# Performance work log

Hardware: AMD Instinct MI355X
Metric: run time of the kernel (lower is better)

Reference implementation:

```python
import jax, jax.numpy as jnp
import numpy as np
import math

NUM_HEADS = 8
HEAD_SIZE = 32

def get_alibi_slopes(n_heads):
    def pow2_slopes(n):
        start = 2.0 ** (-2.0 ** (-(math.log2(n) - 3)))
        ratio = start
        return [start * ratio ** i for i in range(n)]
    if math.log2(n_heads).is_integer():
        return np.array(pow2_slopes(n_heads), dtype=np.float32)
    cp2 = 2 ** math.floor(math.log2(n_heads))
    extra = pow2_slopes(2 * cp2)[0::2][: n_heads - cp2]
    return np.array(pow2_slopes(cp2) + extra, dtype=np.float32)

ALIBI_SLOPES = jnp.asarray(get_alibi_slopes(NUM_HEADS))  # [H]

def setup_inputs() -> dict:
    key = jax.random.key(0)
    ks = jax.random.split(key, 6)
    B, T, C = 32, 512, 256
    s = 1.0 / math.sqrt(C)
    return {
        "x": jax.random.normal(ks[0], (B, T, C), dtype=jnp.float32),
        "Wq": jax.random.normal(ks[1], (C, NUM_HEADS * HEAD_SIZE), dtype=jnp.float32) * s,
        "Wk": jax.random.normal(ks[2], (C, NUM_HEADS * HEAD_SIZE), dtype=jnp.float32) * s,
        "Wv": jax.random.normal(ks[3], (C, NUM_HEADS * HEAD_SIZE), dtype=jnp.float32) * s,
        "Wo": jax.random.normal(ks[4], (NUM_HEADS * HEAD_SIZE, C), dtype=jnp.float32) * s,
        "bo": jax.random.normal(ks[5], (C,), dtype=jnp.float32) * 0.01,
    }

def reference(x, Wq, Wk, Wv, Wo, bo):
    # Faithful eval-mode forward (dropout disabled) of the torch MultiHeadAttention.
    B, T, C = x.shape
    H, D = NUM_HEADS, HEAD_SIZE
    q = (x @ Wq).reshape(B, T, H, D).transpose(0, 2, 1, 3)  # [B,H,T,D]
    k = (x @ Wk).reshape(B, T, H, D).transpose(0, 2, 1, 3)
    v = (x @ Wv).reshape(B, T, H, D).transpose(0, 2, 1, 3)
    scale = 1.0 / math.sqrt(D)
    wei = jnp.einsum("bhtd,bhsd->bhts", q, k) * scale  # [B,H,T,T]
    pos = jnp.arange(T)
    rel = (pos[None, :] - pos[:, None]).astype(jnp.float32)  # bias[i,j] = j - i
    bias = ALIBI_SLOPES[:, None, None] * rel[None, :, :]      # [H,T,T]
    wei = wei + bias[None]
    causal = pos[None, :] <= pos[:, None]  # [T,T], True where j <= i
    wei = jnp.where(causal[None, None], wei, -jnp.inf)
    wei = jax.nn.softmax(wei, axis=-1)
    out = jnp.einsum("bhts,bhsd->bhtd", wei, v)  # [B,H,T,D]
    out = out.transpose(0, 2, 1, 3).reshape(B, T, H * D)
    return out @ Wo + bo
```

## Files before the change

### kernel.cpp

```cpp
#include <hip/hip_runtime.h>
#include <stdint.h>

#define LOG2E 1.4426950408889634f

typedef __attribute__((ext_vector_type(8))) short bf16x8;
typedef __attribute__((ext_vector_type(4))) float f32x4;

__device__ __forceinline__ unsigned short f2bf(float f) {
  union { float f; unsigned int u; } v; v.f = f;
  unsigned int u = v.u;
  u += 0x7FFFu + ((u >> 16) & 1u);
  return (unsigned short)(u >> 16);
}

__device__ __forceinline__ unsigned int cvt_pk_bf16(float lo, float hi) {
  unsigned int r;
  asm("v_cvt_pk_bf16_f32 %0, %1, %2" : "=v"(r) : "v"(lo), "v"(hi));
  return r;
}

__global__ void cvt_f32_bf16(const float* __restrict__ src, unsigned short* __restrict__ dst, int n4) {
  int i = blockIdx.x * blockDim.x + threadIdx.x;
  if (i < n4) {
    float4 v = reinterpret_cast<const float4*>(src)[i];
    ushort4 o;
    o.x = f2bf(v.x); o.y = f2bf(v.y); o.z = f2bf(v.z); o.w = f2bf(v.w);
    reinterpret_cast<ushort4*>(dst)[i] = o;
  }
}

struct WPtrs { const float* src[4]; unsigned short* dst[4]; };
__global__ void transpose_w(WPtrs p) {
  __shared__ float tile[32][33];
  const float* src = p.src[blockIdx.z];
  unsigned short* dst = p.dst[blockIdx.z];
  int x = blockIdx.x * 32 + threadIdx.x;
  int y = blockIdx.y * 32 + threadIdx.y;
  #pragma unroll
  for (int j = 0; j < 32; j += 8)
    tile[threadIdx.y + j][threadIdx.x] = src[(y + j) * 256 + x];
  __syncthreads();
  int xo = blockIdx.y * 32 + threadIdx.x;
  int yo = blockIdx.x * 32 + threadIdx.y;
  #pragma unroll
  for (int j = 0; j < 32; j += 8)
    dst[(yo + j) * 256 + xo] = f2bf(tile[threadIdx.x][threadIdx.y + j]);
}

template<int MODE>
__launch_bounds__(256, 2)
__global__ void gemm128(const unsigned short* __restrict__ A,
                        const unsigned short* __restrict__ Wt,
                        unsigned short* __restrict__ q_out,
                        unsigned short* __restrict__ k_out,
                        unsigned short* __restrict__ vT,
                        const float* __restrict__ bo,
                        float* __restrict__ f_out) {
  __shared__ unsigned short As[128][72];
  __shared__ unsigned short Bs[128][72];
  const int tid = threadIdx.x;
  const int m0 = blockIdx.x * 128;
  int wsel, n0;
  if (MODE == 0) { wsel = blockIdx.y >> 1; n0 = (blockIdx.y & 1) * 128; }
  else           { wsel = 0;               n0 = blockIdx.y * 128; }
  const unsigned short* W = Wt + wsel * 65536;
  const int w = tid >> 6, lane = tid & 63;
  const int wm = (w >> 1) * 64, wn = (w & 1) * 64;
  const int lr = lane & 15, lg = lane >> 4;

  f32x4 acc[4][4] = {};

  for (int kt = 0; kt < 4; ++kt) {
    #pragma unroll
    for (int cc = 0; cc < 4; ++cc) {
      int c = tid + cc * 256;
      int row = c >> 3, col = (c & 7) * 8;
      *reinterpret_cast<int4*>(&As[row][col]) =
        *reinterpret_cast<const int4*>(&A[(size_t)(m0 + row) * 256 + kt * 64 + col]);
      *reinterpret_cast<int4*>(&Bs[row][col]) =
        *reinterpret_cast<const int4*>(&W[(size_t)(n0 + row) * 256 + kt * 64 + col]);
    }
    __syncthreads();
    #pragma unroll
    for (int kk = 0; kk < 2; ++kk) {
      bf16x8 af[4], bfr[4];
      #pragma unroll
      for (int mf = 0; mf < 4; ++mf)
        af[mf] = *reinterpret_cast<const bf16x8*>(&As[wm + mf * 16 + lr][kk * 32 + lg * 8]);
      #pragma unroll
      for (int nf = 0; nf < 4; ++nf)
        bfr[nf] = *reinterpret_cast<const bf16x8*>(&Bs[wn + nf * 16 + lr][kk * 32 + lg * 8]);
      #pragma unroll
      for (int mf = 0; mf < 4; ++mf)
        #pragma unroll
        for (int nf = 0; nf < 4; ++nf)
          acc[mf][nf] = __builtin_amdgcn_mfma_f32_16x16x32_bf16(af[mf], bfr[nf], acc[mf][nf], 0, 0, 0);
    }
    __syncthreads();
  }

  if (MODE == 0) {
    if (wsel < 2) {
      unsigned short* dst = (wsel == 0) ? q_out : k_out;
      #pragma unroll
      for (int mf = 0; mf < 4; ++mf)
        #pragma unroll
        for (int nf = 0; nf < 4; ++nf)
          #pragma unroll
          for (int r = 0; r < 4; ++r)
            dst[(size_t)(m0 + wm + mf * 16 + lg * 4 + r) * 256 + (n0 + wn + nf * 16 + lr)] =
              f2bf(acc[mf][nf][r]);
    } else {
      #pragma unroll
      for (int mf = 0; mf < 4; ++mf)
        #pragma unroll
        for (int nf = 0; nf < 4; ++nf) {
          int ncol = n0 + wn + nf * 16 + lr;
          int h = ncol >> 5, d = ncol & 31;
          int m = m0 + wm + mf * 16 + lg * 4;
          int b = m >> 9, t = m & 511;
          ushort4 pk;
          pk.x = f2bf(acc[mf][nf][0]); pk.y = f2bf(acc[mf][nf][1]);
          pk.z = f2bf(acc[mf][nf][2]); pk.w = f2bf(acc[mf][nf][3]);
          *reinterpret_cast<ushort4*>(&vT[((size_t)((b * 8 + h) * 32 + d)) * 512 + t]) = pk;
        }
    }
  } else {
    #pragma unroll
    for (int mf = 0; mf < 4; ++mf)
      #pragma unroll
      for (int nf = 0; nf < 4; ++nf)
        #pragma unroll
        for (int r = 0; r < 4; ++r) {
          int ncol = n0 + wn + nf * 16 + lr;
          f_out[(size_t)(m0 + wm + mf * 16 + lg * 4 + r) * 256 + ncol] = acc[mf][nf][r] + bo[ncol];
        }
  }
}

__launch_bounds__(256, 2)
__global__ void attn_k(const unsigned short* __restrict__ qb,
                       const unsigned short* __restrict__ kb,
                       const unsigned short* __restrict__ vT,
                       unsigned short* __restrict__ ob) {
  extern __shared__ unsigned short smem[];
  unsigned short* Ks = smem;
  unsigned short* Vs = smem + 16384;
  unsigned short* Pl = smem + 32768;
  const int p = blockIdx.x, h = blockIdx.y, b = blockIdx.z;
  const int tid = threadIdx.x, wv = tid >> 6, lane = tid & 63;
  const int lr = lane & 15, lg = lane >> 4;

  {
    const unsigned short* ksrc = kb + ((size_t)b * 512) * 256 + h * 32;
    #pragma unroll
    for (int it = 0; it < 8; ++it) {
      int idx = tid + it * 256;
      int row = idx >> 2, g = idx & 3;
      *reinterpret_cast<int4*>(&Ks[row * 32 + g * 8]) =
        *reinterpret_cast<const int4*>(&ksrc[(size_t)row * 256 + g * 8]);
    }
    const unsigned short* vsrc = vT + ((size_t)(b * 8 + h) * 32) * 512;
    #pragma unroll
    for (int it = 0; it < 8; ++it) {
      int idx = tid + it * 256;
      int d = idx >> 6, cg = idx & 63;
      int col = (cg * 8) ^ ((d & 7) << 3);
      *reinterpret_cast<int4*>(&Vs[d * 512 + col]) =
        *reinterpret_cast<const int4*>(&vsrc[(size_t)d * 512 + cg * 8]);
    }
  }
  __syncthreads();

  const float scale2 = 0.17677669529663687f * LOG2E;
  const float slope2 = exp2f(-(float)(h + 1)) * LOG2E;
  float cc[16];
  #pragma unroll
  for (int t = 0; t < 4; ++t)
    #pragma unroll
    for (int r = 0; r < 4; ++r) cc[t * 4 + r] = slope2 * (float)(t * 16 + r);

  char* Plw = (char*)(Pl) + wv * 2048;
  const int swz = (lr & 7) << 4;

  for (int i = 0; i < 4; ++i) {
    const int c = p + 2 * (wv + 4 * i);
    const int qq = c * 16;
    bf16x8 qf = *reinterpret_cast<const bf16x8*>(
        &qb[((size_t)(b * 512 + qq + lr)) * 256 + h * 32 + lg * 8]);
    float m = -1e30f, l = 0.f;
    f32x4 oT0 = {0.f, 0.f, 0.f, 0.f}, oT1 = {0.f, 0.f, 0.f, 0.f};
    const int nsteps = c / 4 + 1;
    const int nfull = (qq >= 63) ? ((qq - 63) / 64 + 1) : 0;
    const float bb0 = slope2 * (float)(lg * 4 - lr - qq);

    for (int s = 0; s < nsteps; ++s) {
      const int kb0 = s * 64;
      f32x4 sv[4];
      #pragma unroll
      for (int t = 0; t < 4; ++t) {
        bf16x8 kf = *reinterpret_cast<const bf16x8*>(&Ks[(kb0 + t * 16 + lr) * 32 + lg * 8]);
        f32x4 z = {0.f, 0.f, 0.f, 0.f};
        sv[t] = __builtin_amdgcn_mfma_f32_16x16x32_bf16(kf, qf, z, 0, 0, 0);
      }
      float bb = bb0 + slope2 * (float)kb0;
      float x[16];
      #pragma unroll
      for (int t = 0; t < 4; ++t)
        #pragma unroll
        for (int r = 0; r < 4; ++r)
          x[t * 4 + r] = sv[t][r] * scale2 + (bb + cc[t * 4 + r]);
      if (s >= nfull) {
        int thr = qq + lr - kb0 - lg * 4;
        #pragma unroll
        for (int t = 0; t < 4; ++t)
          #pragma unroll
          for (int r = 0; r < 4; ++r)
            x[t * 4 + r] = ((t * 16 + r) <= thr) ? x[t * 4 + r] : -1e30f;
      }
      float bm = x[0];
      #pragma unroll
      for (int j = 1; j < 16; ++j) bm = fmaxf(bm, x[j]);
      bm = fmaxf(bm, __shfl_xor(bm, 16));
      bm = fmaxf(bm, __shfl_xor(bm, 32));
      float mn = fmaxf(m, bm);
      float alpha = __builtin_amdgcn_exp2f(m - mn);
      m = mn;
      l *= alpha;
      #pragma unroll
      for (int r = 0; r < 4; ++r) { oT0[r] *= alpha; oT1[r] *= alpha; }
      float ps = 0.f;
      #pragma unroll
      for (int j = 0; j < 16; ++j) { x[j] = __builtin_amdgcn_exp2f(x[j] - m); ps += x[j]; }
      l += ps;
      #pragma unroll
      for (int t = 0; t < 4; ++t)
        #pragma unroll
        for (int pp = 0; pp < 2; ++pp) {
          unsigned int w2 = cvt_pk_bf16(x[t * 4 + 2 * pp], x[t * 4 + 2 * pp + 1]);
          int cbyte = (t * 32 + lg * 8 + pp * 4) ^ swz;
          *reinterpret_cast<unsigned int*>(Plw + lr * 128 + cbyte) = w2;
        }
      #pragma unroll
      for (int ks = 0; ks < 2; ++ks) {
        int cb = (ks * 64 + lg * 16) ^ swz;
        bf16x8 pb = *reinterpret_cast<const bf16x8*>(Plw + lr * 128 + cb);
        #pragma unroll
        for (int dt = 0; dt < 2; ++dt) {
          int d = dt * 16 + lr;
          int col = (kb0 + ks * 32 + lg * 8) ^ ((d & 7) << 3);
          bf16x8 vf = *reinterpret_cast<const bf16x8*>(&Vs[d * 512 + col]);
          if (dt == 0) oT0 = __builtin_amdgcn_mfma_f32_16x16x32_bf16(vf, pb, oT0, 0, 0, 0);
          else         oT1 = __builtin_amdgcn_mfma_f32_16x16x32_bf16(vf, pb, oT1, 0, 0, 0);
        }
      }
    }
    l += __shfl_xor(l, 16);
    l += __shfl_xor(l, 32);
    float inv = 1.0f / l;
    unsigned int w0 = cvt_pk_bf16(oT0[0] * inv, oT0[1] * inv);
    unsigned int w1 = cvt_pk_bf16(oT0[2] * inv, oT0[3] * inv);
    unsigned int w2 = cvt_pk_bf16(oT1[0] * inv, oT1[1] * inv);
    unsigned int w3 = cvt_pk_bf16(oT1[2] * inv, oT1[3] * inv);
    size_t obase = ((size_t)(b * 512 + qq + lr)) * 256 + h * 32;
    *reinterpret_cast<uint2*>(&ob[obase + lg * 4]) = make_uint2(w0, w1);
    *reinterpret_cast<uint2*>(&ob[obase + 16 + lg * 4]) = make_uint2(w2, w3);
  }
}

extern "C" void kernel_launch(void* const* d_in, const int* in_sizes, int n_in,
                              void* d_out, int out_size, void* d_ws, size_t ws_size,
                              hipStream_t stream) {
  const float* x  = (const float*)d_in[0];
  const float* Wq = (const float*)d_in[1];
  const float* Wk = (const float*)d_in[2];
  const float* Wv = (const float*)d_in[3];
  const float* Wo = (const float*)d_in[4];
  const float* bo = (const float*)d_in[5];
  float* out = (float*)d_out;

  char* ws = (char*)d_ws;
  unsigned short* xb = (unsigned short*)(ws);
  unsigned short* qb = (unsigned short*)(ws + (8u  << 20));
  unsigned short* kb = (unsigned short*)(ws + (16u << 20));
  unsigned short* vT = (unsigned short*)(ws + (24u << 20));
  unsigned short* wt = (unsigned short*)(ws + (32u << 20));
  unsigned short* ob = xb;

  cvt_f32_bf16<<<4096, 256, 0, stream>>>(x, xb, 1048576);

  WPtrs p;
  p.src[0] = Wq; p.src[1] = Wk; p.src[2] = Wv; p.src[3] = Wo;
  p.dst[0] = wt; p.dst[1] = wt + 65536; p.dst[2] = wt + 2 * 65536; p.dst[3] = wt + 3 * 65536;
  transpose_w<<<dim3(8, 8, 4), dim3(32, 8), 0, stream>>>(p);

  gemm128<0><<<dim3(128, 6), 256, 0, stream>>>(xb, wt, qb, kb, vT, nullptr, nullptr);
  attn_k<<<dim3(2, 8, 32), 256, 73728, stream>>>(qb, kb, vT, ob);
  gemm128<1><<<dim3(128, 2), 256, 0, stream>>>(ob, wt + 3 * 65536, nullptr, nullptr, nullptr, bo, out);
}
```

Measured before the change: 63.64 us.

## Fuse x conversion into QKV GEMM, interleave attention chunks, swizzle K tiles

Removes the separate fp32-to-bf16 conversion kernel for x and converts inside the QKV GEMM tile load, saving one launch and one round trip of x through global memory. The attention kernel now gives each wave four query chunks paired so their causal lengths balance (g, 15-g, 16+g, 31-g) and steps them together, so multiple independent chains are in flight. K rows are stored in LDS with an XOR swizzle to cut bank conflicts, and the GEMM launch bounds rise to 3 blocks per CU. Keeping four chunk states live raises register pressure, and the QKV GEMM now reads fp32 x, doubling its A-tile global traffic.

```diff
diff --git a/kernel.cpp b/kernel.cpp
--- a/kernel.cpp
+++ b/kernel.cpp
@@ -17,16 +17,6 @@
   unsigned int r;
   asm("v_cvt_pk_bf16_f32 %0, %1, %2" : "=v"(r) : "v"(lo), "v"(hi));
   return r;
-}
-
-__global__ void cvt_f32_bf16(const float* __restrict__ src, unsigned short* __restrict__ dst, int n4) {
-  int i = blockIdx.x * blockDim.x + threadIdx.x;
-  if (i < n4) {
-    float4 v = reinterpret_cast<const float4*>(src)[i];
-    ushort4 o;
-    o.x = f2bf(v.x); o.y = f2bf(v.y); o.z = f2bf(v.z); o.w = f2bf(v.w);
-    reinterpret_cast<ushort4*>(dst)[i] = o;
-  }
 }
 
 struct WPtrs { const float* src[4]; unsigned short* dst[4]; };
@@ -48,8 +38,9 @@
 }
 
 template<int MODE>
-__launch_bounds__(256, 2)
-__global__ void gemm128(const unsigned short* __restrict__ A,
+__launch_bounds__(256, 3)
+__global__ void gemm128(const float* __restrict__ Ax,
+                        const unsigned short* __restrict__ Ab,
                         const unsigned short* __restrict__ Wt,
                         unsigned short* __restrict__ q_out,
                         unsigned short* __restrict__ k_out,
@@ -74,11 +65,21 @@
     #pragma unroll
     for (int cc = 0; cc < 4; ++cc) {
       int c = tid + cc * 256;
-      int row = c >> 3, col = (c & 7) * 8;
-      *reinterpret_cast<int4*>(&As[row][col]) =
-        *reinterpret_cast<const int4*>(&A[(size_t)(m0 + row) * 256 + kt * 64 + col]);
-      *reinterpret_cast<int4*>(&Bs[row][col]) =
-        *reinterpret_cast<const int4*>(&W[(size_t)(n0 + row) * 256 + kt * 64 + col]);
+      int row = c >> 3, colg = c & 7;
+      if constexpr (MODE == 0) {
+        const float* s = &Ax[(size_t)(m0 + row) * 256 + kt * 64 + colg * 8];
+        float4 f0 = *reinterpret_cast<const float4*>(s);
+        float4 f1 = *reinterpret_cast<const float4*>(s + 4);
+        uint4 pk;
+        pk.x = cvt_pk_bf16(f0.x, f0.y); pk.y = cvt_pk_bf16(f0.z, f0.w);
+        pk.z = cvt_pk_bf16(f1.x, f1.y); pk.w = cvt_pk_bf16(f1.z, f1.w);
+        *reinterpret_cast<uint4*>(&As[row][colg * 8]) = pk;
+      } else {
+        *reinterpret_cast<int4*>(&As[row][colg * 8]) =
+          *reinterpret_cast<const int4*>(&Ab[(size_t)(m0 + row) * 256 + kt * 64 + colg * 8]);
+      }
+      *reinterpret_cast<int4*>(&Bs[row][colg * 8]) =
+        *reinterpret_cast<const int4*>(&W[(size_t)(n0 + row) * 256 + kt * 64 + colg * 8]);
     }
     __syncthreads();
     #pragma unroll
@@ -138,15 +139,112 @@
   }
 }
 
+struct CSt {
+  bf16x8 qf;
+  f32x4 o0, o1;
+  float m, l, bb0;
+  int nfull, qq;
+};
+
+__device__ __forceinline__ void attn_init(CSt& st, int c, const unsigned short* qb,
+    int b, int h, int lr, int lg, float slope2) {
+  st.qq = c * 16;
+  st.qf = *reinterpret_cast<const bf16x8*>(
+      &qb[(size_t)(b * 512 + st.qq + lr) * 256 + h * 32 + lg * 8]);
+  f32x4 z = {0.f, 0.f, 0.f, 0.f};
+  st.o0 = z; st.o1 = z;
+  st.m = -1e30f; st.l = 0.f;
+  st.nfull = (st.qq >= 63) ? ((st.qq - 63) / 64 + 1) : 0;
+  st.bb0 = slope2 * (float)(lg * 4 - lr - st.qq);
+}
+
+__device__ __forceinline__ void attn_step(CSt& st, int s,
+    const unsigned short* __restrict__ Ks, const unsigned short* __restrict__ Vs,
+    char* __restrict__ Pw, int lr, int lg, float scale2, float slope2,
+    const float* cc, int swz) {
+  const int kb0 = s * 64;
+  const int kchunk = (lg ^ ((lr >> 1) & 3)) * 8;
+  f32x4 sv[4];
+  #pragma unroll
+  for (int t = 0; t < 4; ++t) {
+    bf16x8 kf = *reinterpret_cast<const bf16x8*>(&Ks[(kb0 + t * 16 + lr) * 32 + kchunk]);
+    f32x4 z = {0.f, 0.f, 0.f, 0.f};
+    sv[t] = __builtin_amdgcn_mfma_f32_16x16x32_bf16(kf, st.qf, z, 0, 0, 0);
+  }
+  float bb = st.bb0 + slope2 * (float)kb0;
+  float x[16];
+  #pragma unroll
+  for (int t = 0; t < 4; ++t)
+    #pragma unroll
+    for (int r = 0; r < 4; ++r)
+      x[t * 4 + r] = sv[t][r] * scale2 + (bb + cc[t * 4 + r]);
+  if (s >= st.nfull) {
+    int thr = st.qq + lr - kb0 - lg * 4;
+    #pragma unroll
+    for (int t = 0; t < 4; ++t)
+      #pragma unroll
+      for (int r = 0; r < 4; ++r)
+        x[t * 4 + r] = ((t * 16 + r) <= thr) ? x[t * 4 + r] : -1e30f;
+  }
+  float bm = x[0];
+  #pragma unroll
+  for (int j = 1; j < 16; ++j) bm = fmaxf(bm, x[j]);
+  bm = fmaxf(bm, __shfl_xor(bm, 16));
+  bm = fmaxf(bm, __shfl_xor(bm, 32));
+  float mn = fmaxf(st.m, bm);
+  float alpha = __builtin_amdgcn_exp2f(st.m - mn);
+  st.m = mn;
+  st.l *= alpha;
+  #pragma unroll
+  for (int r = 0; r < 4; ++r) { st.o0[r] *= alpha; st.o1[r] *= alpha; }
+  float ps = 0.f;
+  #pragma unroll
+  for (int j = 0; j < 16; ++j) { x[j] = __builtin_amdgcn_exp2f(x[j] - mn); ps += x[j]; }
+  st.l += ps;
+  char* Prow = Pw + lr * 128;
+  #pragma unroll
+  for (int t = 0; t < 4; ++t)
+    #pragma unroll
+    for (int pp = 0; pp < 2; ++pp) {
+      unsigned int w2 = cvt_pk_bf16(x[t * 4 + 2 * pp], x[t * 4 + 2 * pp + 1]);
+      *reinterpret_cast<unsigned int*>(Prow + ((t * 32 + lg * 8 + pp * 4) ^ swz)) = w2;
+    }
+  #pragma unroll
+  for (int ks = 0; ks < 2; ++ks) {
+    bf16x8 pb = *reinterpret_cast<const bf16x8*>(Prow + ((ks * 64 + lg * 16) ^ swz));
+    #pragma unroll
+    for (int dt = 0; dt < 2; ++dt) {
+      int col = (kb0 + ks * 32 + lg * 8) ^ ((lr & 7) << 3);
+      bf16x8 vf = *reinterpret_cast<const bf16x8*>(&Vs[(dt * 16 + lr) * 512 + col]);
+      if (dt == 0) st.o0 = __builtin_amdgcn_mfma_f32_16x16x32_bf16(vf, pb, st.o0, 0, 0, 0);
+      else         st.o1 = __builtin_amdgcn_mfma_f32_16x16x32_bf16(vf, pb, st.o1, 0, 0, 0);
+    }
+  }
+}
+
+__device__ __forceinline__ void attn_fin(CSt& st, unsigned short* __restrict__ ob,
+                                         int b, int h, int lr, int lg) {
+  float l = st.l;
+  l += __shfl_xor(l, 16);
+  l += __shfl_xor(l, 32);
+  float inv = 1.0f / l;
+  unsigned int w0 = cvt_pk_bf16(st.o0[0] * inv, st.o0[1] * inv);
+  unsigned int w1 = cvt_pk_bf16(st.o0[2] * inv, st.o0[3] * inv);
+  unsigned int w2 = cvt_pk_bf16(st.o1[0] * inv, st.o1[1] * inv);
+  unsigned int w3 = cvt_pk_bf16(st.o1[2] * inv, st.o1[3] * inv);
+  size_t obase = (size_t)(b * 512 + st.qq + lr) * 256 + h * 32;
+  *reinterpret_cast<uint2*>(&ob[obase + lg * 4]) = make_uint2(w0, w1);
+  *reinterpret_cast<uint2*>(&ob[obase + 16 + lg * 4]) = make_uint2(w2, w3);
+}
+
 __launch_bounds__(256, 2)
 __global__ void attn_k(const unsigned short* __restrict__ qb,
                        const unsigned short* __restrict__ kb,
                        const unsigned short* __restrict__ vT,
                        unsigned short* __restrict__ ob) {
-  extern __shared__ unsigned short smem[];
-  unsigned short* Ks = smem;
-  unsigned short* Vs = smem + 16384;
-  unsigned short* Pl = smem + 32768;
+  __shared__ unsigned short Ks[512 * 32];
+  __shared__ unsigned short Vs[32 * 512];
+  __shared__ char Pb[8192];
   const int p = blockIdx.x, h = blockIdx.y, b = blockIdx.z;
   const int tid = threadIdx.x, wv = tid >> 6, lane = tid & 63;
   const int lr = lane & 15, lg = lane >> 4;
@@ -157,7 +255,8 @@
     for (int it = 0; it < 8; ++it) {
       int idx = tid + it * 256;
       int row = idx >> 2, g = idx & 3;
-      *reinterpret_cast<int4*>(&Ks[row * 32 + g * 8]) =
+      int gs = g ^ ((row >> 1) & 3);
+      *reinterpret_cast<int4*>(&Ks[row * 32 + gs * 8]) =
         *reinterpret_cast<const int4*>(&ksrc[(size_t)row * 256 + g * 8]);
     }
     const unsigned short* vsrc = vT + ((size_t)(b * 8 + h) * 32) * 512;
@@ -179,93 +278,29 @@
   for (int t = 0; t < 4; ++t)
     #pragma unroll
     for (int r = 0; r < 4; ++r) cc[t * 4 + r] = slope2 * (float)(t * 16 + r);
-
-  char* Plw = (char*)(Pl) + wv * 2048;
   const int swz = (lr & 7) << 4;
-
-  for (int i = 0; i < 4; ++i) {
-    const int c = p + 2 * (wv + 4 * i);
-    const int qq = c * 16;
-    bf16x8 qf = *reinterpret_cast<const bf16x8*>(
-        &qb[((size_t)(b * 512 + qq + lr)) * 256 + h * 32 + lg * 8]);
-    float m = -1e30f, l = 0.f;
-    f32x4 oT0 = {0.f, 0.f, 0.f, 0.f}, oT1 = {0.f, 0.f, 0.f, 0.f};
-    const int nsteps = c / 4 + 1;
-    const int nfull = (qq >= 63) ? ((qq - 63) / 64 + 1) : 0;
-    const float bb0 = slope2 * (float)(lg * 4 - lr - qq);
-
-    for (int s = 0; s < nsteps; ++s) {
-      const int kb0 = s * 64;
-      f32x4 sv[4];
-      #pragma unroll
-      for (int t = 0; t < 4; ++t) {
-        bf16x8 kf = *reinterpret_cast<const bf16x8*>(&Ks[(kb0 + t * 16 + lr) * 32 + lg * 8]);
-        f32x4 z = {0.f, 0.f, 0.f, 0.f};
-        sv[t] = __builtin_amdgcn_mfma_f32_16x16x32_bf16(kf, qf, z, 0, 0, 0);
-      }
-      float bb = bb0 + slope2 * (float)kb0;
-      float x[16];
-      #pragma unroll
-      for (int t = 0; t < 4; ++t)
-        #pragma unroll
-        for (int r = 0; r < 4; ++r)
-          x[t * 4 + r] = sv[t][r] * scale2 + (bb + cc[t * 4 + r]);
-      if (s >= nfull) {
-        int thr = qq + lr - kb0 - lg * 4;
-        #pragma unroll
-        for (int t = 0; t < 4; ++t)
-          #pragma unroll
-          for (int r = 0; r < 4; ++r)
-            x[t * 4 + r] = ((t * 16 + r) <= thr) ? x[t * 4 + r] : -1e30f;
-      }
-      float bm = x[0];
-      #pragma unroll
-      for (int j = 1; j < 16; ++j) bm = fmaxf(bm, x[j]);
-      bm = fmaxf(bm, __shfl_xor(bm, 16));
-      bm = fmaxf(bm, __shfl_xor(bm, 32));
-      float mn = fmaxf(m, bm);
-      float alpha = __builtin_amdgcn_exp2f(m - mn);
-      m = mn;
-      l *= alpha;
-      #pragma unroll
-      for (int r = 0; r < 4; ++r) { oT0[r] *= alpha; oT1[r] *= alpha; }
-      float ps = 0.f;
-      #pragma unroll
-      for (int j = 0; j < 16; ++j) { x[j] = __builtin_amdgcn_exp2f(x[j] - m); ps += x[j]; }
-      l += ps;
-      #pragma unroll
-      for (int t = 0; t < 4; ++t)
-        #pragma unroll
-        for (int pp = 0; pp < 2; ++pp) {
-          unsigned int w2 = cvt_pk_bf16(x[t * 4 + 2 * pp], x[t * 4 + 2 * pp + 1]);
-          int cbyte = (t * 32 + lg * 8 + pp * 4) ^ swz;
-          *reinterpret_cast<unsigned int*>(Plw + lr * 128 + cbyte) = w2;
-        }
-      #pragma unroll
-      for (int ks = 0; ks < 2; ++ks) {
-        int cb = (ks * 64 + lg * 16) ^ swz;
-        bf16x8 pb = *reinterpret_cast<const bf16x8*>(Plw + lr * 128 + cb);
-        #pragma unroll
-        for (int dt = 0; dt < 2; ++dt) {
-          int d = dt * 16 + lr;
-          int col = (kb0 + ks * 32 + lg * 8) ^ ((d & 7) << 3);
-          bf16x8 vf = *reinterpret_cast<const bf16x8*>(&Vs[d * 512 + col]);
-          if (dt == 0) oT0 = __builtin_amdgcn_mfma_f32_16x16x32_bf16(vf, pb, oT0, 0, 0, 0);
-          else         oT1 = __builtin_amdgcn_mfma_f32_16x16x32_bf16(vf, pb, oT1, 0, 0, 0);
-        }
-      }
-    }
-    l += __shfl_xor(l, 16);
-    l += __shfl_xor(l, 32);
-    float inv = 1.0f / l;
-    unsigned int w0 = cvt_pk_bf16(oT0[0] * inv, oT0[1] * inv);
-    unsigned int w1 = cvt_pk_bf16(oT0[2] * inv, oT0[3] * inv);
-    unsigned int w2 = cvt_pk_bf16(oT1[0] * inv, oT1[1] * inv);
-    unsigned int w3 = cvt_pk_bf16(oT1[2] * inv, oT1[3] * inv);
-    size_t obase = ((size_t)(b * 512 + qq + lr)) * 256 + h * 32;
-    *reinterpret_cast<uint2*>(&ob[obase + lg * 4]) = make_uint2(w0, w1);
-    *reinterpret_cast<uint2*>(&ob[obase + 16 + lg * 4]) = make_uint2(w2, w3);
-  }
+  char* Pw = Pb + wv * 2048;
+
+  const int g = p * 4 + wv;
+  const int c0 = g, c1 = 15 - g, c2 = 16 + g, c3 = 31 - g;
+  CSt s0, s1, s2, s3;
+  attn_init(s0, c0, qb, b, h, lr, lg, slope2);
+  attn_init(s1, c1, qb, b, h, lr, lg, slope2);
+  attn_init(s2, c2, qb, b, h, lr, lg, slope2);
+  attn_init(s3, c3, qb, b, h, lr, lg, slope2);
+  const int n0 = c0 / 4 + 1, n1 = c1 / 4 + 1, n2 = c2 / 4 + 1, n3 = c3 / 4 + 1;
+
+  for (int s = 0; s < n3; ++s) {
+    if (s < n0) attn_step(s0, s, Ks, Vs, Pw, lr, lg, scale2, slope2, cc, swz);
+    if (s < n1) attn_step(s1, s, Ks, Vs, Pw, lr, lg, scale2, slope2, cc, swz);
+    if (s < n2) attn_step(s2, s, Ks, Vs, Pw, lr, lg, scale2, slope2, cc, swz);
+    attn_step(s3, s, Ks, Vs, Pw, lr, lg, scale2, slope2, cc, swz);
+  }
+
+  attn_fin(s0, ob, b, h, lr, lg);
+  attn_fin(s1, ob, b, h, lr, lg);
+  attn_fin(s2, ob, b, h, lr, lg);
+  attn_fin(s3, ob, b, h, lr, lg);
 }
 
 extern "C" void kernel_launch(void* const* d_in, const int* in_sizes, int n_in,
@@ -280,21 +315,18 @@
   float* out = (float*)d_out;
 
   char* ws = (char*)d_ws;
-  unsigned short* xb = (unsigned short*)(ws);
-  unsigned short* qb = (unsigned short*)(ws + (8u  << 20));
-  unsigned short* kb = (unsigned short*)(ws + (16u << 20));
-  unsigned short* vT = (unsigned short*)(ws + (24u << 20));
+  unsigned short* qb = (unsigned short*)(ws);
+  unsigned short* kb = (unsigned short*)(ws + (8u  << 20));
+  unsigned short* vT = (unsigned short*)(ws + (16u << 20));
+  unsigned short* ob = (unsigned short*)(ws + (24u << 20));
   unsigned short* wt = (unsigned short*)(ws + (32u << 20));
-  unsigned short* ob = xb;
-
-  cvt_f32_bf16<<<4096, 256, 0, stream>>>(x, xb, 1048576);
 
   WPtrs p;
   p.src[0] = Wq; p.src[1] = Wk; p.src[2] = Wv; p.src[3] = Wo;
   p.dst[0] = wt; p.dst[1] = wt + 65536; p.dst[2] = wt + 2 * 65536; p.dst[3] = wt + 3 * 65536;
   transpose_w<<<dim3(8, 8, 4), dim3(32, 8), 0, stream>>>(p);
 
-  gemm128<0><<<dim3(128, 6), 256, 0, stream>>>(xb, wt, qb, kb, vT, nullptr, nullptr);
-  attn_k<<<dim3(2, 8, 32), 256, 73728, stream>>>(qb, kb, vT, ob);
-  gemm128<1><<<dim3(128, 2), 256, 0, stream>>>(ob, wt + 3 * 65536, nullptr, nullptr, nullptr, bo, out);
-}
+  gemm128<0><<<dim3(128, 6), 256, 0, stream>>>(x, nullptr, wt, qb, kb, vT, nullptr, nullptr);
+  attn_k<<<dim3(2, 8, 32), 256, 0, stream>>>(qb, kb, vT, ob);
+  gemm128<1><<<dim3(128, 2), 256, 0, stream>>>(nullptr, ob, wt + 3 * 65536, nullptr, nullptr, nullptr, bo, out);
+}
```

New measurement: 58.46 us. -8.1%, faster.
